# Optimization experiments

Hardware: AMD Instinct MI355X
Metric: run time of the kernel (lower is better)

The kernel has to match this reference:

```python
import jax, jax.numpy as jnp
import numpy as np

IOU_THRESH = 0.5  # standard positive-match threshold used by the repo's match()


def _make_boxes(key, shape):
    """Random valid [x1,y1,x2,y2] boxes in a ~1000px image."""
    k1, k2 = jax.random.split(key)
    c = jax.random.uniform(k1, shape + (2,), minval=0.0, maxval=1000.0)
    s = jax.random.uniform(k2, shape + (2,), minval=20.0, maxval=200.0)
    return jnp.concatenate([c - s / 2, c + s / 2], axis=-1)


def setup_inputs() -> dict:
    key = jax.random.key(0)
    ks = jax.random.split(key, 6)
    N, L, M, C = 32, 4096, 128, 80
    gt_boxes = _make_boxes(ks[0], (N, M))
    rois = _make_boxes(ks[1], (N, L))
    # make the first M rois jittered copies of gt so every image has positives
    jitter = jax.random.normal(ks[2], (N, M, 4)) * 2.0
    rois = rois.at[:, :M, :].set(gt_boxes + jitter)
    cls_scores = jax.random.normal(ks[3], (N, L, C), dtype=jnp.float32)
    bbox_deltas = jax.random.normal(ks[4], (N, L, 4 * C), dtype=jnp.float32)
    gt_clses = jax.random.randint(ks[5], (N, M), 0, C, dtype=jnp.int64)
    return dict(rois=rois, cls_scores=cls_scores, bbox_deltas=bbox_deltas,
                gt_boxes=gt_boxes, gt_clses=gt_clses)


def _pairwise_iou(rois, gt):
    # rois [N,L,4], gt [N,M,4] -> iou [N,L,M]
    lt = jnp.maximum(rois[:, :, None, :2], gt[:, None, :, :2])
    rb = jnp.minimum(rois[:, :, None, 2:], gt[:, None, :, 2:])
    wh = jnp.clip(rb - lt, 0.0)
    inter = wh[..., 0] * wh[..., 1]
    area_r = (rois[..., 2] - rois[..., 0]) * (rois[..., 3] - rois[..., 1])
    area_g = (gt[..., 2] - gt[..., 0]) * (gt[..., 3] - gt[..., 1])
    return inter / (area_r[:, :, None] + area_g[:, None, :] - inter)


def reference(rois, cls_scores, bbox_deltas, gt_boxes, gt_clses):
    N, L, C = cls_scores.shape
    # 1) per-class bbox_delta gather (vectorized version of the N*L python loop)
    score_idxs = jnp.argmax(cls_scores, axis=2)                    # [N,L]
    deltas4 = bbox_deltas.reshape(N, L, C, 4)
    chosen = jnp.take_along_axis(deltas4, score_idxs[:, :, None, None],
                                 axis=2).squeeze(2)                # [N,L,4]
    # 2) IoU match (pred = rois, as in original)
    iou = _pairwise_iou(rois, gt_boxes)                            # [N,L,M]
    best = jnp.argmax(iou, axis=2)                                 # [N,L]
    max_iou = jnp.max(iou, axis=2)
    pos = max_iou >= IOU_THRESH                                    # [N,L]
    labels = jnp.take_along_axis(gt_clses, best, axis=1)           # [N,L]
    # 3) balanced sampling: per class, keep the first ceil(max(1, n_pos/ncls))
    #    positives in roi-index order (matches idxs[:sample_num] in balance())
    onehot = jax.nn.one_hot(labels, C, dtype=jnp.float32) * pos[..., None].astype(jnp.float32)
    cum = jnp.cumsum(onehot, axis=1)                               # count incl. self
    rank = jnp.take_along_axis(cum - onehot, labels[..., None], axis=2).squeeze(2)
    n_pos = pos.sum(axis=1).astype(jnp.float32)                    # [N]
    sample_num = jnp.ceil(jnp.maximum(1.0, n_pos / C))             # [N]
    select = pos & (rank < sample_num[:, None])                    # [N,L]
    # 4) per-image mean CrossEntropy over selected samples, summed over images
    logp = jax.nn.log_softmax(cls_scores, axis=-1)
    nll = -jnp.take_along_axis(logp, labels[..., None], axis=2).squeeze(2)
    sel = select.astype(cls_scores.dtype)
    per_img = (sel * nll).sum(axis=1) / sel.sum(axis=1)
    cls_loss = per_img.sum()
    # keep the (otherwise-dead) class-specific delta gather alive, value-neutral
    cls_loss = cls_loss + 0.0 * chosen.sum()
    return cls_loss
```

## Files before the change

### kernel.cpp

```cpp
#include <hip/hip_runtime.h>
#include <math.h>

#define N_IMG 32
#define L_ROI 4096
#define M_GT  128
#define C_CLS 80
#define NSEG  16
#define BLK_PER_IMG 5

__global__ __launch_bounds__(256) void k_match(
    const float4* __restrict__ rois,
    const float4* __restrict__ gt_boxes,
    const int*    __restrict__ gt_cls,
    int* __restrict__ plist,
    int* __restrict__ cnt,
    int* __restrict__ arr1,
    int* __restrict__ arr2)
{
    __shared__ float4 sgt[M_GT];
    __shared__ float  sarea[M_GT];
    __shared__ int    swt[4];

    const int n   = blockIdx.x >> 4;
    const int seg = blockIdx.x & 15;
    const int t   = threadIdx.x;
    if (blockIdx.x == 0) {
        if (t < N_IMG) arr1[t] = 0;
        if (t == N_IMG) *arr2 = 0;
    }
    if (t < M_GT) {
        float4 g = gt_boxes[n * M_GT + t];
        sgt[t]   = g;
        sarea[t] = (g.z - g.x) * (g.w - g.y);
    }
    __syncthreads();

    const int l = seg * 256 + t;
    float4 r = rois[(size_t)n * L_ROI + l];
    float ar = (r.z - r.x) * (r.w - r.y);

    float ib = -1.0f;
    float db =  1.0f;
    int   bi =  0;
    #pragma unroll 8
    for (int m = 0; m < M_GT; ++m) {
        float4 g = sgt[m];
        float ix = fminf(r.z, g.z) - fmaxf(r.x, g.x);
        float iy = fminf(r.w, g.w) - fmaxf(r.y, g.y);
        ix = fmaxf(ix, 0.0f);
        iy = fmaxf(iy, 0.0f);
        float inter = ix * iy;
        float den   = ar + sarea[m] - inter;
        if (inter * db > ib * den) { ib = inter; db = den; bi = m; }
    }
    const int pos  = (ib + ib >= db) ? 1 : 0;
    const int lab  = gt_cls[n * M_GT + bi];
    const int lane = t & 63;
    const int wv   = t >> 6;

    unsigned long long mask = __ballot(pos);
    if (lane == 0) swt[wv] = (int)__popcll(mask);
    __syncthreads();
    int woff = 0;
    for (int w = 0; w < wv; ++w) woff += swt[w];
    if (pos) {
        int pref = (int)__popcll(mask & ((1ull << lane) - 1ull));
        plist[((n * NSEG + seg) << 8) + woff + pref] = (l << 7) | lab;
    }
    if (t == 0) cnt[n * NSEG + seg] = swt[0] + swt[1] + swt[2] + swt[3];
}

__global__ __launch_bounds__(1024) void k_selnll(
    const float* __restrict__ cls_scores,
    const int*   __restrict__ plist,
    const int*   __restrict__ cnt,
    float* __restrict__ pnll,
    int*   __restrict__ pcnt,
    int*   __restrict__ arr1,
    int*   __restrict__ arr2,
    float* __restrict__ per_img,
    float* __restrict__ out)
{
    __shared__ float bnll[16];
    __shared__ int   bcnt[16];

    const int b    = blockIdx.x;
    const int t    = threadIdx.x;
    const int lane = t & 63;
    const int wv   = t >> 6;
    const int n    = b / BLK_PER_IMG;
    const int c    = (b % BLK_PER_IMG) * 16 + wv;

    const int segcnt = (lane < NSEG) ? cnt[n * NSEG + lane] : 0;
    int incl = segcnt;
    #pragma unroll
    for (int o = 1; o < NSEG; o <<= 1) {
        int y = __shfl_up(incl, o);
        if (lane >= o) incl += y;
    }
    const int np = __shfl(incl, NSEG - 1);
    const int sn = max(1, (np + C_CLS - 1) / C_CLS);
    const int* pl = plist + ((size_t)n << 12);

    float lsum = 0.0f;
    int taken = 0;
    for (int base = 0; base < np && taken < sn; base += 64) {
        const int g = base + lane;
        int seg = 0;
        #pragma unroll
        for (int bit = 8; bit; bit >>= 1) {
            const int cand = seg + bit;
            if (cand <= 15 && __shfl(incl, cand - 1) <= g) seg = cand;
        }
        const int st = __shfl(incl, seg) - __shfl(segcnt, seg);
        const int e  = (g < np) ? pl[(seg << 8) + (g - st)] : -1;

        unsigned long long m = __ballot(e >= 0 && (e & 127) == c);
        while (m && taken < sn) {
            const int src = __ffsll(m) - 1;
            m &= m - 1;
            const int roi = __shfl(e, src) >> 7;

            const float* rp = cls_scores + ((size_t)n * L_ROI + roi) * C_CLS;
            float v0 = rp[lane];
            float v1 = (lane < C_CLS - 64) ? rp[64 + lane] : -INFINITY;
            float mx = fmaxf(v0, v1);
            #pragma unroll
            for (int o = 32; o; o >>= 1) mx = fmaxf(mx, __shfl_xor(mx, o));
            float sm = expf(v0 - mx) + ((lane < C_CLS - 64) ? expf(v1 - mx) : 0.0f);
            #pragma unroll
            for (int o = 32; o; o >>= 1) sm += __shfl_xor(sm, o);
            const float logZ = mx + logf(sm);
            const float sc = (c < 64) ? __shfl(v0, c) : __shfl(v1, c - 64);
            lsum += logZ - sc;
            ++taken;
        }
    }
    if (lane == 0) { bnll[wv] = lsum; bcnt[wv] = taken; }
    __syncthreads();

    if (t == 0) {
        float v = 0.0f;
        int   q = 0;
        #pragma unroll
        for (int j = 0; j < 16; ++j) { v += bnll[j]; q += bcnt[j]; }
        pnll[b] = v;
        pcnt[b] = q;
        int tk = __hip_atomic_fetch_add(&arr1[n], 1, __ATOMIC_ACQ_REL,
                                        __HIP_MEMORY_SCOPE_AGENT);
        if (tk == BLK_PER_IMG - 1) {
            __threadfence();
            float vv = 0.0f;
            int   qq = 0;
            #pragma unroll
            for (int j = 0; j < BLK_PER_IMG; ++j) {
                vv += pnll[n * BLK_PER_IMG + j];
                qq += pcnt[n * BLK_PER_IMG + j];
            }
            per_img[n] = vv / (float)qq;
            int tk2 = __hip_atomic_fetch_add(arr2, 1, __ATOMIC_ACQ_REL,
                                             __HIP_MEMORY_SCOPE_AGENT);
            if (tk2 == N_IMG - 1) {
                __threadfence();
                float tot = 0.0f;
                #pragma unroll 4
                for (int i = 0; i < N_IMG; ++i) tot += per_img[i];
                out[0] = tot;
            }
        }
    }
}

extern "C" void kernel_launch(void* const* d_in, const int* in_sizes, int n_in,
                              void* d_out, int out_size, void* d_ws, size_t ws_size,
                              hipStream_t stream) {
    const float4* rois       = (const float4*)d_in[0];
    const float*  cls_scores = (const float*)d_in[1];
    const float4* gt_boxes   = (const float4*)d_in[3];
    const int*    gt_clses   = (const int*)d_in[4];
    float* out = (float*)d_out;

    char* ws = (char*)d_ws;
    int*   arr1    = (int*)(ws + 0);
    int*   arr2    = (int*)(ws + 128);
    int*   cnt     = (int*)(ws + 256);
    float* pnll    = (float*)(ws + 4096);
    int*   pcnt    = (int*)(ws + 8192);
    float* per_img = (float*)(ws + 12288);
    int*   plist   = (int*)(ws + 32768);

    k_match<<<N_IMG * NSEG, 256, 0, stream>>>(
        rois, gt_boxes, gt_clses, plist, cnt, arr1, arr2);
    k_selnll<<<N_IMG * BLK_PER_IMG, 1024, 0, stream>>>(
        cls_scores, plist, cnt, pnll, pcnt, arr1, arr2, per_img, out);
}
```

Before: 32.93 us.

## Stage positive list in LDS and process two selected ROIs per iteration

The selection kernel now copies the image's compacted positive list from its global segments into a contiguous LDS array, with one wavefront per segment, using a prefix table computed once. This replaces the per-iteration binary search over segment offsets and the scattered global loads. The NLL loop also pulls two matching ROIs at a time so their cls_scores row loads can overlap before the reductions. In exchange it adds 16KB of LDS per block and two block barriers, and the copy is paid even when each wave needs only a few samples.

```diff
diff --git a/kernel.cpp b/kernel.cpp
--- a/kernel.cpp
+++ b/kernel.cpp
@@ -81,6 +81,8 @@
     float* __restrict__ per_img,
     float* __restrict__ out)
 {
+    __shared__ int   ldslist[L_ROI];
+    __shared__ int   spref[NSEG + 1];
     __shared__ float bnll[16];
     __shared__ int   bcnt[16];
 
@@ -91,49 +93,80 @@
     const int n    = b / BLK_PER_IMG;
     const int c    = (b % BLK_PER_IMG) * 16 + wv;
 
-    const int segcnt = (lane < NSEG) ? cnt[n * NSEG + lane] : 0;
-    int incl = segcnt;
-    #pragma unroll
-    for (int o = 1; o < NSEG; o <<= 1) {
-        int y = __shfl_up(incl, o);
-        if (lane >= o) incl += y;
-    }
-    const int np = __shfl(incl, NSEG - 1);
+    if (wv == 0) {
+        int v = (lane < NSEG) ? cnt[n * NSEG + lane] : 0;
+        int incl = v;
+        #pragma unroll
+        for (int o = 1; o < NSEG; o <<= 1) {
+            int y = __shfl_up(incl, o);
+            if (lane >= o) incl += y;
+        }
+        if (lane < NSEG) spref[lane] = incl - v;
+        if (lane == NSEG - 1) spref[NSEG] = incl;
+    }
+    __syncthreads();
+
+    {
+        const int base = spref[wv];
+        const int segc = spref[wv + 1] - base;
+        const int* src = plist + (((size_t)n << 4) + wv << 8);
+        for (int i = lane; i < segc; i += 64) ldslist[base + i] = src[i];
+    }
+    __syncthreads();
+
+    const int np = spref[NSEG];
     const int sn = max(1, (np + C_CLS - 1) / C_CLS);
-    const int* pl = plist + ((size_t)n << 12);
 
     float lsum = 0.0f;
     int taken = 0;
     for (int base = 0; base < np && taken < sn; base += 64) {
-        const int g = base + lane;
-        int seg = 0;
-        #pragma unroll
-        for (int bit = 8; bit; bit >>= 1) {
-            const int cand = seg + bit;
-            if (cand <= 15 && __shfl(incl, cand - 1) <= g) seg = cand;
-        }
-        const int st = __shfl(incl, seg) - __shfl(segcnt, seg);
-        const int e  = (g < np) ? pl[(seg << 8) + (g - st)] : -1;
-
+        const int e = (base + lane < np) ? ldslist[base + lane] : -1;
         unsigned long long m = __ballot(e >= 0 && (e & 127) == c);
         while (m && taken < sn) {
-            const int src = __ffsll(m) - 1;
+            const int s0 = __ffsll(m) - 1;
             m &= m - 1;
-            const int roi = __shfl(e, src) >> 7;
-
-            const float* rp = cls_scores + ((size_t)n * L_ROI + roi) * C_CLS;
-            float v0 = rp[lane];
-            float v1 = (lane < C_CLS - 64) ? rp[64 + lane] : -INFINITY;
-            float mx = fmaxf(v0, v1);
-            #pragma unroll
-            for (int o = 32; o; o >>= 1) mx = fmaxf(mx, __shfl_xor(mx, o));
-            float sm = expf(v0 - mx) + ((lane < C_CLS - 64) ? expf(v1 - mx) : 0.0f);
-            #pragma unroll
-            for (int o = 32; o; o >>= 1) sm += __shfl_xor(sm, o);
-            const float logZ = mx + logf(sm);
-            const float sc = (c < 64) ? __shfl(v0, c) : __shfl(v1, c - 64);
-            lsum += logZ - sc;
-            ++taken;
+            const int roi0 = __shfl(e, s0) >> 7;
+            int roi1 = -1;
+            if (m && taken + 1 < sn) {
+                const int s1 = __ffsll(m) - 1;
+                m &= m - 1;
+                roi1 = __shfl(e, s1) >> 7;
+            }
+
+            const float* rp0 = cls_scores + ((size_t)n * L_ROI + roi0) * C_CLS;
+            float a0 = rp0[lane];
+            float a1 = (lane < C_CLS - 64) ? rp0[64 + lane] : -INFINITY;
+            float b0 = 0.0f, b1 = -INFINITY;
+            if (roi1 >= 0) {
+                const float* rp1 = cls_scores + ((size_t)n * L_ROI + roi1) * C_CLS;
+                b0 = rp1[lane];
+                b1 = (lane < C_CLS - 64) ? rp1[64 + lane] : -INFINITY;
+            }
+
+            {
+                float mx = fmaxf(a0, a1);
+                #pragma unroll
+                for (int o = 32; o; o >>= 1) mx = fmaxf(mx, __shfl_xor(mx, o));
+                float sm = expf(a0 - mx) + ((lane < C_CLS - 64) ? expf(a1 - mx) : 0.0f);
+                #pragma unroll
+                for (int o = 32; o; o >>= 1) sm += __shfl_xor(sm, o);
+                const float logZ = mx + logf(sm);
+                const float sc = (c < 64) ? __shfl(a0, c) : __shfl(a1, c - 64);
+                lsum += logZ - sc;
+                ++taken;
+            }
+            if (roi1 >= 0) {
+                float mx = fmaxf(b0, b1);
+                #pragma unroll
+                for (int o = 32; o; o >>= 1) mx = fmaxf(mx, __shfl_xor(mx, o));
+                float sm = expf(b0 - mx) + ((lane < C_CLS - 64) ? expf(b1 - mx) : 0.0f);
+                #pragma unroll
+                for (int o = 32; o; o >>= 1) sm += __shfl_xor(sm, o);
+                const float logZ = mx + logf(sm);
+                const float sc = (c < 64) ? __shfl(b0, c) : __shfl(b1, c - 64);
+                lsum += logZ - sc;
+                ++taken;
+            }
         }
     }
     if (lane == 0) { bnll[wv] = lsum; bcnt[wv] = taken; }
```

After: 32.43 us. No clear change (-1.5%).
